# Optimization experiments

Hardware: AMD Instinct MI355X
Metric: run time of the kernel (lower is better)

Reference implementation:

```python
import jax, jax.numpy as jnp
import numpy as np

NUM_REL = 6
EMBED_DIM = 128
B, N = 8, 1024


def _relation_type(dx, dy):
    # Faithful to _get_relation_type's if/elif chain (order matters).
    return jnp.select(
        [dy > 0.5,
         dy < -0.5,
         dx < -0.5,
         dx > 0.5,
         (jnp.abs(dx) < 0.3) & (jnp.abs(dy) < 0.3)],
        [0, 1, 2, 3, 4],
        5,
    )


def setup_inputs() -> dict:
    key = jax.random.key(0)
    k1, k2, k3, k4 = jax.random.split(key, 4)
    symbols = jax.random.normal(k1, (B, N, EMBED_DIM), dtype=jnp.float32)
    positions = jax.random.normal(k2, (B, N, 2), dtype=jnp.float32)
    # 6 Linear(embed_dim, embed_dim) layers, stacked: W [6, D, D] (torch layout: y = x @ W.T + b)
    bound = 1.0 / np.sqrt(EMBED_DIM)
    W = jax.random.uniform(k3, (NUM_REL, EMBED_DIM, EMBED_DIM), dtype=jnp.float32,
                           minval=-bound, maxval=bound)
    b = jax.random.uniform(k4, (NUM_REL, EMBED_DIM), dtype=jnp.float32,
                           minval=-bound, maxval=bound)
    return {"symbols": symbols, "positions": positions, "W": W, "b": b}


def reference(symbols, positions, W, b):
    Bn, Nn, D = symbols.shape
    # dx[b,i,j] = pos[b,j,0] - pos[b,i,0]; dy likewise (source i -> target j)
    dx = positions[:, None, :, 0] - positions[:, :, None, 0]  # [B, i, j]
    dy = positions[:, None, :, 1] - positions[:, :, None, 1]
    rel = _relation_type(dx, dy)  # [B, i, j] in {0..5}

    # Per-type transform of every source symbol: T[r,b,i,:] = symbols[b,i] @ W[r].T + b[r]
    T = jnp.einsum('bid,red->rbie', symbols, W) + b[:, None, None, :]  # [6, B, N, D]

    # One-hot relation mask with i != j excluded; scatter-add into targets j.
    not_diag = ~jnp.eye(Nn, dtype=bool)  # [i, j]
    mask = (rel[None] == jnp.arange(NUM_REL)[:, None, None, None]) & not_diag  # [6, B, i, j]
    agg = jnp.einsum('rbij,rbie->bje', mask.astype(symbols.dtype), T)  # [B, N, D]
    return symbols + agg
```

## Files before the change

### kernel.cpp

```cpp
#include <hip/hip_runtime.h>
#include <stdint.h>


typedef __attribute__((ext_vector_type(8))) short bf16x8;
typedef __attribute__((ext_vector_type(4))) float f32x4;
union U4B { uint4 u; bf16x8 b; };

#if defined(__has_builtin)
#  if __has_builtin(__builtin_amdgcn_global_load_lds)
#    define HAVE_GLL 1
#  endif
#  if __has_builtin(__builtin_amdgcn_mul_u24)
#    define OH_MUL24 1
#  endif
#endif

__device__ __forceinline__ uint16_t f2bf(float f) {
    union { float f; uint32_t u; } v; v.f = f;
    uint32_t u = v.u;
    uint32_t r = (u + 0x7FFFu + ((u >> 16) & 1u)) >> 16;
    return (uint16_t)r;
}

#define BARRIER_LGKM() do {                                   \
    asm volatile("s_waitcnt lgkmcnt(0)" ::: "memory");        \
    __builtin_amdgcn_s_barrier();                             \
    asm volatile("" ::: "memory");                            \
} while (0)

__global__ __launch_bounds__(256)
void prep_kernel(const float* __restrict__ X, const float* __restrict__ W,
                 uint16_t* __restrict__ symT, uint16_t* __restrict__ WtB,
                 float* __restrict__ T4) {
    const int blk = blockIdx.x, tid = threadIdx.x;
    if (blk < 256) {
        __shared__ float T[64 * 65];
        const int b = blk & 7, z = blk >> 3, it = z & 15, et = z >> 4;
        const int i0 = it * 64, e0 = et * 64;
        const float4* Xf = (const float4*)X;
#pragma unroll
        for (int s = 0; s < 4; ++s) {
            int il = s * 16 + (tid >> 4), e4 = tid & 15;
            float4 v = Xf[((size_t)b << 15) + (size_t)((i0 + il) << 5) + (e0 >> 2) + e4];
            T[il * 65 + e4 * 4 + 0] = v.x;
            T[il * 65 + e4 * 4 + 1] = v.y;
            T[il * 65 + e4 * 4 + 2] = v.z;
            T[il * 65 + e4 * 4 + 3] = v.w;
        }
        __syncthreads();
#pragma unroll
        for (int s = 0; s < 4; ++s) {
            int el = s * 16 + (tid >> 4), il4 = tid & 15;
            uint16_t h0 = f2bf(T[(il4 * 4 + 0) * 65 + el]);
            uint16_t h1 = f2bf(T[(il4 * 4 + 1) * 65 + el]);
            uint16_t h2 = f2bf(T[(il4 * 4 + 2) * 65 + el]);
            uint16_t h3 = f2bf(T[(il4 * 4 + 3) * 65 + el]);
            uint2 pk = { (uint32_t)h0 | ((uint32_t)h1 << 16),
                         (uint32_t)h2 | ((uint32_t)h3 << 16) };
            *(uint2*)&symT[((size_t)b << 17) + ((size_t)(e0 + el) << 10) + i0 + il4 * 4] = pk;
        }
    } else if (blk < 352) {
        int g = (blk - 256) * 256 + tid;
        float4 v = ((const float4*)W)[g];
        int r = g >> 12, rem = g & 4095, ep = rem >> 5, e4 = rem & 31;
        int kb = r * 4 + (e4 >> 3);
        int kc = (e4 & 7) * 4;
        uint16_t h0 = f2bf(v.x), h1 = f2bf(v.y), h2 = f2bf(v.z), h3 = f2bf(v.w);
        uint2 pk = { (uint32_t)h0 | ((uint32_t)h1 << 16),
                     (uint32_t)h2 | ((uint32_t)h3 << 16) };
        *(uint2*)&WtB[((size_t)(kb * 128 + ep)) * 32 + kc] = pk;
    } else {
        const int z = blk - 352, bb = z >> 2, qq = z & 3;
        const int e = tid & 127, half = tid >> 7;
        const float* base = X + (((size_t)(bb << 10) + (qq << 8) + (half << 7)) << 7) + e;
        float s = 0.f;
#pragma unroll 8
        for (int itr = 0; itr < 128; ++itr) s += base[(size_t)itr << 7];
        __shared__ float red[256];
        red[tid] = s;
        __syncthreads();
        if (tid < 128) T4[(z << 7) + tid] = red[tid] + red[tid + 128];
    }
}

#define SP 776

__global__ __launch_bounds__(512, 4)
void fused_kernel(const float* __restrict__ sym, const float* __restrict__ pos,
                  const uint16_t* __restrict__ symT, const uint16_t* __restrict__ WtB,
                  const float* __restrict__ bias, const float* __restrict__ T4,
                  float* __restrict__ out) {
    __shared__ __align__(16) char smem[81920];
    uint16_t* symTS   = (uint16_t*)smem;
    float2*   posS    = (float2*)(smem + 32768);
    uint16_t* SA      = (uint16_t*)smem;
    float*    partial = (float*)(smem + 24832);
    uint32_t* rel32   = (uint32_t*)(smem + 65536);

    const int blk = blockIdx.x;
    const int b = blk & 7, jt = blk >> 3, j0 = jt * 16;
    const int tid = threadIdx.x;
    const int w = tid >> 6, lane = tid & 63, m = lane & 15, q = lane >> 4;

    const uint16_t* symTb = symT + ((size_t)b << 17);

    int goff[4];
#pragma unroll
    for (int s = 0; s < 4; ++s) {
        int e = (w << 4) + (s << 2) + (lane >> 4);
        int sg = (lane & 15) ^ (e & 15);
        goff[s] = (e << 10) + (sg << 3);
    }
    const int lwb = w << 12;

    auto issue_chunk = [&](int cidx, int bufsel) {
#ifdef HAVE_GLL
#pragma unroll
        for (int s = 0; s < 4; ++s) {
            const uint16_t* gp = symTb + goff[s] + cidx * 128;
            char* lp = smem + bufsel * 32768 + lwb + s * 1024;
            typedef const __attribute__((address_space(1))) uint32_t gu32;
            typedef __attribute__((address_space(3))) uint32_t lu32;
            __builtin_amdgcn_global_load_lds((gu32*)gp, (lu32*)lp, 16, 0, 0);
        }
#else
#pragma unroll
        for (int s = 0; s < 4; ++s) {
            uint4 v = *(const uint4*)(symTb + goff[s] + cidx * 128);
            *(uint4*)(smem + bufsel * 32768 + lwb + s * 1024 + lane * 16) = v;
        }
#endif
    };

    const float2* pos2 = (const float2*)pos + ((size_t)b << 10);
    float2 p0 = pos2[tid], p1 = pos2[tid + 512];
    issue_chunk(0, 0);
    posS[tid] = p0;
    posS[tid + 512] = p1;
    BARRIER_LGKM();

    {
        const int mm = tid & 15, grp = tid >> 4;
        const int j = j0 + mm;
        const float2 pj = posS[j];
        uint32_t* dst = &rel32[mm * 256];
        const int sw = mm * 2;
#pragma unroll
        for (int s = 0; s < 8; ++s) {
            uint32_t word = 0;
#pragma unroll
            for (int qq = 0; qq < 4; ++qq) {
                int i = grp * 32 + s * 4 + qq;
                float2 pi = posS[i];
                float dx = pj.x - pi.x, dy = pj.y - pi.y;
                int r = (dy > 0.5f) ? 0
                      : (dy < -0.5f) ? 1
                      : (dx < -0.5f) ? 2
                      : (dx > 0.5f)  ? 3
                      : (fabsf(dx) < 0.3f && fabsf(dy) < 0.3f) ? 4
                      : 5;
                uint32_t oh = (i == j) ? 0u : (1u << r);
                word |= oh << (8 * qq);
            }
            dst[(grp * 8 + s) ^ sw] = word;
        }
    }
    BARRIER_LGKM();

    f32x4 acc[5];
#pragma unroll
    for (int r = 0; r < 5; ++r) acc[r] = (f32x4){0.f, 0.f, 0.f, 0.f};

    const int E = (w << 4) + m;
    const int esw = m;
    const int csw = m * 2;

    for (int c = 0; c < 8; ++c) {
        if (c < 7) {
            issue_chunk(c + 1, (c + 1) & 1);
            asm volatile("s_waitcnt vmcnt(4)" ::: "memory");
        } else {
            asm volatile("s_waitcnt vmcnt(0)" ::: "memory");
        }
        const uint16_t* bt = symTS + ((c & 1) << 14) + E * 128;
        const uint32_t* crow = &rel32[m * 256 + c * 32];
#pragma unroll
        for (int ks = 0; ks < 4; ++ks) {
            U4B bfr;
            bfr.u = *(const uint4*)(bt + ((((ks << 2) + q) ^ esw) << 3));
            uint2 cw = *(const uint2*)&crow[(((ks << 3) + (q << 1)) ^ csw)];
            uint32_t hx01 = __builtin_amdgcn_perm(cw.x, cw.x, 0x01010000u) & 0x00FF00FFu;
            uint32_t hx23 = __builtin_amdgcn_perm(cw.x, cw.x, 0x03030202u) & 0x00FF00FFu;
            uint32_t hy01 = __builtin_amdgcn_perm(cw.y, cw.y, 0x01010000u) & 0x00FF00FFu;
            uint32_t hy23 = __builtin_amdgcn_perm(cw.y, cw.y, 0x03030202u) & 0x00FF00FFu;
#pragma unroll
            for (int r = 0; r < 5; ++r) {
                const uint32_t rm = 0x00010001u << r;
                U4B a;
#ifdef OH_MUL24
                const uint32_t mc = 0x3F80u >> r;
                a.u.x = (uint32_t)__builtin_amdgcn_mul_u24((int)(hx01 & rm), (int)mc);
                a.u.y = (uint32_t)__builtin_amdgcn_mul_u24((int)(hx23 & rm), (int)mc);
                a.u.z = (uint32_t)__builtin_amdgcn_mul_u24((int)(hy01 & rm), (int)mc);
                a.u.w = (uint32_t)__builtin_amdgcn_mul_u24((int)(hy23 & rm), (int)mc);
#else
                uint32_t g2;
                g2 = hx01 & rm; a.u.x = (g2 << (14 - r)) - (g2 << (7 - r));
                g2 = hx23 & rm; a.u.y = (g2 << (14 - r)) - (g2 << (7 - r));
                g2 = hy01 & rm; a.u.z = (g2 << (14 - r)) - (g2 << (7 - r));
                g2 = hy23 & rm; a.u.w = (g2 << (14 - r)) - (g2 << (7 - r));
#endif
                acc[r] = __builtin_amdgcn_mfma_f32_16x16x32_bf16(a.b, bfr.b, acc[r], 0, 0, 0);
            }
        }
    }
    BARRIER_LGKM();

#pragma unroll
    for (int r = 0; r < 5; ++r)
#pragma unroll
        for (int reg = 0; reg < 4; ++reg)
            SA[(q * 4 + reg) * SP + r * 128 + E] = f2bf(acc[r][reg]);
    {
        float ts = T4[((b << 2) + 0) * 128 + E] + T4[((b << 2) + 1) * 128 + E]
                 + T4[((b << 2) + 2) * 128 + E] + T4[((b << 2) + 3) * 128 + E];
#pragma unroll
        for (int reg = 0; reg < 4; ++reg) {
            float symj = sym[((size_t)((b << 10) + j0 + (q << 2) + reg) << 7) + E];
            float s5 = ts - symj
                     - acc[0][reg] - acc[1][reg] - acc[2][reg] - acc[3][reg] - acc[4][reg];
            SA[(q * 4 + reg) * SP + 5 * 128 + E] = f2bf(s5);
        }
    }
    BARRIER_LGKM();

    {
        const int g = w >> 1, h = w & 1;
        f32x4 c2[4];
#pragma unroll
        for (int nf = 0; nf < 4; ++nf) c2[nf] = (f32x4){0.f, 0.f, 0.f, 0.f};
#pragma unroll
        for (int kf = 0; kf < 6; ++kf) {
            U4B af;
            af.u = *(const uint4*)&SA[m * SP + g * 192 + kf * 32 + q * 8];
            const int kb = g * 6 + kf;
#pragma unroll
            for (int nf = 0; nf < 4; ++nf) {
                U4B bw;
                bw.u = *(const uint4*)&WtB[((size_t)(kb * 128 + h * 64 + nf * 16 + m)) * 32 + q * 8];
                c2[nf] = __builtin_amdgcn_mfma_f32_16x16x32_bf16(af.b, bw.b, c2[nf], 0, 0, 0);
            }
        }
#pragma unroll
        for (int nf = 0; nf < 4; ++nf)
#pragma unroll
            for (int reg = 0; reg < 4; ++reg)
                partial[g * 2112 + (q * 4 + reg) * 132 + h * 64 + nf * 16 + m] = c2[nf][reg];
    }
    BARRIER_LGKM();

    {
        const int j = tid >> 5, t = tid & 31, e0 = t << 2;
        const uint32_t* row = &rel32[j * 256 + t * 8];
        uint32_t s0 = 0, s1 = 0, s2 = 0, s3 = 0, s4 = 0;
#pragma unroll
        for (int k = 0; k < 8; ++k) {
            uint32_t wd = row[k];
            s0 += wd & 0x01010101u;        s1 += (wd >> 1) & 0x01010101u;
            s2 += (wd >> 2) & 0x01010101u; s3 += (wd >> 3) & 0x01010101u;
            s4 += (wd >> 4) & 0x01010101u;
        }
        int cnt[6];
        cnt[0] = (int)((s0 * 0x01010101u) >> 24);
        cnt[1] = (int)((s1 * 0x01010101u) >> 24);
        cnt[2] = (int)((s2 * 0x01010101u) >> 24);
        cnt[3] = (int)((s3 * 0x01010101u) >> 24);
        cnt[4] = (int)((s4 * 0x01010101u) >> 24);
#pragma unroll
        for (int off = 1; off < 32; off <<= 1)
#pragma unroll
            for (int r = 0; r < 5; ++r)
                cnt[r] += __shfl_xor(cnt[r], off, 64);
        cnt[5] = 1023 - cnt[0] - cnt[1] - cnt[2] - cnt[3] - cnt[4];

        float4 a4 = {0.f, 0.f, 0.f, 0.f};
#pragma unroll
        for (int g4 = 0; g4 < 4; ++g4) {
            float4 u = *(const float4*)&partial[g4 * 2112 + j * 132 + e0];
            a4.x += u.x; a4.y += u.y; a4.z += u.z; a4.w += u.w;
        }
#pragma unroll
        for (int r = 0; r < 6; ++r) {
            float cf = (float)cnt[r];
            float4 bb = *(const float4*)&bias[r * 128 + e0];
            a4.x += cf * bb.x; a4.y += cf * bb.y; a4.z += cf * bb.z; a4.w += cf * bb.w;
        }
        size_t o = ((size_t)(b * 1024 + j0 + j) << 7) + e0;
        float4 sv = *(const float4*)&sym[o];
        float4 ov = { sv.x + a4.x, sv.y + a4.y, sv.z + a4.z, sv.w + a4.w };
        *(float4*)&out[o] = ov;
    }
}

extern "C" void kernel_launch(void* const* d_in, const int* in_sizes, int n_in,
                              void* d_out, int out_size, void* d_ws, size_t ws_size,
                              hipStream_t stream) {
    const float* symbols   = (const float*)d_in[0];
    const float* positions = (const float*)d_in[1];
    const float* W         = (const float*)d_in[2];
    const float* bias      = (const float*)d_in[3];
    float* out             = (float*)d_out;

    char* ws = (char*)d_ws;
    uint16_t* symT = (uint16_t*)ws;
    uint16_t* WtB  = (uint16_t*)(ws + 2097152);
    float*    T4   = (float*)(ws + 2097152 + 196608);

    prep_kernel<<<384, 256, 0, stream>>>(symbols, W, symT, WtB, T4);
    fused_kernel<<<512, 512, 0, stream>>>(symbols, positions, symT, WtB, bias, T4, out);
}
```

Baseline: 94.00 us.

## Precompute one-hot A fragments in shared memory and halve K-chunk size

Moves the one-hot relation-mask expansion out of the MFMA inner loop. Each chunk's bf16 A fragments are now built once per block into a double-buffered LDS region, instead of every wave redundantly expanding them from packed bytes. The K loop is split into 16 chunks of 64 rows rather than 8 chunks of 128, with a new XOR swizzle, and the total shared memory footprint shrinks. In exchange, every chunk now ends with a block-wide barrier and the inner loop adds extra LDS reads for the A fragments.

```diff
diff --git a/kernel.cpp b/kernel.cpp
--- a/kernel.cpp
+++ b/kernel.cpp
@@ -90,12 +90,11 @@
                   const uint16_t* __restrict__ symT, const uint16_t* __restrict__ WtB,
                   const float* __restrict__ bias, const float* __restrict__ T4,
                   float* __restrict__ out) {
-    __shared__ __align__(16) char smem[81920];
-    uint16_t* symTS   = (uint16_t*)smem;
+    __shared__ __align__(16) char smem[75008];
     float2*   posS    = (float2*)(smem + 32768);
     uint16_t* SA      = (uint16_t*)smem;
     float*    partial = (float*)(smem + 24832);
-    uint32_t* rel32   = (uint32_t*)(smem + 65536);
+    uint32_t* rel32   = (uint32_t*)(smem + 58624);
 
     const int blk = blockIdx.x;
     const int b = blk & 7, jt = blk >> 3, j0 = jt * 16;
@@ -104,37 +103,79 @@
 
     const uint16_t* symTb = symT + ((size_t)b << 17);
 
-    int goff[4];
-#pragma unroll
-    for (int s = 0; s < 4; ++s) {
-        int e = (w << 4) + (s << 2) + (lane >> 4);
-        int sg = (lane & 15) ^ (e & 15);
-        goff[s] = (e << 10) + (sg << 3);
-    }
-    const int lwb = w << 12;
+    int goff[2];
+#pragma unroll
+    for (int s = 0; s < 2; ++s) {
+        int e = (w << 4) + (s << 3) + (lane >> 3);
+        int t = lane & 7;
+        goff[s] = (e << 10) + ((t ^ (e & 7)) << 3);
+    }
 
     auto issue_chunk = [&](int cidx, int bufsel) {
 #ifdef HAVE_GLL
 #pragma unroll
-        for (int s = 0; s < 4; ++s) {
-            const uint16_t* gp = symTb + goff[s] + cidx * 128;
-            char* lp = smem + bufsel * 32768 + lwb + s * 1024;
+        for (int s = 0; s < 2; ++s) {
+            const uint16_t* gp = symTb + goff[s] + cidx * 64;
+            char* lp = smem + bufsel * 16384 + (w << 11) + (s << 10);
             typedef const __attribute__((address_space(1))) uint32_t gu32;
             typedef __attribute__((address_space(3))) uint32_t lu32;
             __builtin_amdgcn_global_load_lds((gu32*)gp, (lu32*)lp, 16, 0, 0);
         }
 #else
 #pragma unroll
-        for (int s = 0; s < 4; ++s) {
-            uint4 v = *(const uint4*)(symTb + goff[s] + cidx * 128);
-            *(uint4*)(smem + bufsel * 32768 + lwb + s * 1024 + lane * 16) = v;
+        for (int s = 0; s < 2; ++s) {
+            uint4 v = *(const uint4*)(symTb + goff[s] + cidx * 64);
+            *(uint4*)(smem + bufsel * 16384 + (w << 11) + (s << 10) + lane * 16) = v;
         }
 #endif
     };
 
+    const int jx = tid & 15, u16 = (tid >> 4) & 15, rsub = tid >> 8;
+    const int aseg = (u16 >> 1) ^ (jx & 7), ahb = (u16 & 1) * 8;
+
+    auto expandA = [&](int cidx, int bufsel) {
+        uint32_t cw4 = rel32[jx * 256 + (((cidx << 4) + u16) ^ (jx << 1))];
+        uint32_t h01 = __builtin_amdgcn_perm(cw4, cw4, 0x01010000u) & 0x00FF00FFu;
+        uint32_t h23 = __builtin_amdgcn_perm(cw4, cw4, 0x03030202u) & 0x00FF00FFu;
+        char* ab = smem + 32768 + bufsel * 10240;
+        if (rsub == 0) {
+#pragma unroll
+            for (int r = 0; r < 3; ++r) {
+                const uint32_t rm = 0x00010001u << r;
+                uint2 d;
+#ifdef OH_MUL24
+                const uint32_t mc = 0x3F80u >> r;
+                d.x = (uint32_t)__builtin_amdgcn_mul_u24((int)(h01 & rm), (int)mc);
+                d.y = (uint32_t)__builtin_amdgcn_mul_u24((int)(h23 & rm), (int)mc);
+#else
+                uint32_t g2;
+                g2 = h01 & rm; d.x = (g2 << (14 - r)) - (g2 << (7 - r));
+                g2 = h23 & rm; d.y = (g2 << (14 - r)) - (g2 << (7 - r));
+#endif
+                *(uint2*)(ab + (((r * 16 + jx) * 8 + aseg) << 4) + ahb) = d;
+            }
+        } else {
+#pragma unroll
+            for (int r = 3; r < 5; ++r) {
+                const uint32_t rm = 0x00010001u << r;
+                uint2 d;
+#ifdef OH_MUL24
+                const uint32_t mc = 0x3F80u >> r;
+                d.x = (uint32_t)__builtin_amdgcn_mul_u24((int)(h01 & rm), (int)mc);
+                d.y = (uint32_t)__builtin_amdgcn_mul_u24((int)(h23 & rm), (int)mc);
+#else
+                uint32_t g2;
+                g2 = h01 & rm; d.x = (g2 << (14 - r)) - (g2 << (7 - r));
+                g2 = h23 & rm; d.y = (g2 << (14 - r)) - (g2 << (7 - r));
+#endif
+                *(uint2*)(ab + (((r * 16 + jx) * 8 + aseg) << 4) + ahb) = d;
+            }
+        }
+    };
+
+    issue_chunk(0, 0);
     const float2* pos2 = (const float2*)pos + ((size_t)b << 10);
     float2 p0 = pos2[tid], p1 = pos2[tid + 512];
-    issue_chunk(0, 0);
     posS[tid] = p0;
     posS[tid + 512] = p1;
     BARRIER_LGKM();
@@ -167,54 +208,42 @@
     }
     BARRIER_LGKM();
 
+    expandA(0, 0);
+    BARRIER_LGKM();
+
     f32x4 acc[5];
 #pragma unroll
     for (int r = 0; r < 5; ++r) acc[r] = (f32x4){0.f, 0.f, 0.f, 0.f};
 
     const int E = (w << 4) + m;
-    const int esw = m;
-    const int csw = m * 2;
-
-    for (int c = 0; c < 8; ++c) {
-        if (c < 7) {
-            issue_chunk(c + 1, (c + 1) & 1);
-            asm volatile("s_waitcnt vmcnt(4)" ::: "memory");
+    const int bseg0 = q ^ (m & 7);
+    const int bseg1 = (4 + q) ^ (m & 7);
+
+    for (int c = 0; c < 16; ++c) {
+        const int cb = c & 1;
+        if (c < 15) {
+            issue_chunk(c + 1, cb ^ 1);
+            expandA(c + 1, cb ^ 1);
+            asm volatile("s_waitcnt vmcnt(2)" ::: "memory");
         } else {
             asm volatile("s_waitcnt vmcnt(0)" ::: "memory");
         }
-        const uint16_t* bt = symTS + ((c & 1) << 14) + E * 128;
-        const uint32_t* crow = &rel32[m * 256 + c * 32];
-#pragma unroll
-        for (int ks = 0; ks < 4; ++ks) {
+        const char* bb = smem + cb * 16384 + (w << 11) + (m << 7);
+        const char* ab = smem + 32768 + cb * 10240;
+#pragma unroll
+        for (int ks = 0; ks < 2; ++ks) {
             U4B bfr;
-            bfr.u = *(const uint4*)(bt + ((((ks << 2) + q) ^ esw) << 3));
-            uint2 cw = *(const uint2*)&crow[(((ks << 3) + (q << 1)) ^ csw)];
-            uint32_t hx01 = __builtin_amdgcn_perm(cw.x, cw.x, 0x01010000u) & 0x00FF00FFu;
-            uint32_t hx23 = __builtin_amdgcn_perm(cw.x, cw.x, 0x03030202u) & 0x00FF00FFu;
-            uint32_t hy01 = __builtin_amdgcn_perm(cw.y, cw.y, 0x01010000u) & 0x00FF00FFu;
-            uint32_t hy23 = __builtin_amdgcn_perm(cw.y, cw.y, 0x03030202u) & 0x00FF00FFu;
+            bfr.u = *(const uint4*)(bb + ((ks ? bseg1 : bseg0) << 4));
 #pragma unroll
             for (int r = 0; r < 5; ++r) {
-                const uint32_t rm = 0x00010001u << r;
-                U4B a;
-#ifdef OH_MUL24
-                const uint32_t mc = 0x3F80u >> r;
-                a.u.x = (uint32_t)__builtin_amdgcn_mul_u24((int)(hx01 & rm), (int)mc);
-                a.u.y = (uint32_t)__builtin_amdgcn_mul_u24((int)(hx23 & rm), (int)mc);
-                a.u.z = (uint32_t)__builtin_amdgcn_mul_u24((int)(hy01 & rm), (int)mc);
-                a.u.w = (uint32_t)__builtin_amdgcn_mul_u24((int)(hy23 & rm), (int)mc);
-#else
-                uint32_t g2;
-                g2 = hx01 & rm; a.u.x = (g2 << (14 - r)) - (g2 << (7 - r));
-                g2 = hx23 & rm; a.u.y = (g2 << (14 - r)) - (g2 << (7 - r));
-                g2 = hy01 & rm; a.u.z = (g2 << (14 - r)) - (g2 << (7 - r));
-                g2 = hy23 & rm; a.u.w = (g2 << (14 - r)) - (g2 << (7 - r));
-#endif
-                acc[r] = __builtin_amdgcn_mfma_f32_16x16x32_bf16(a.b, bfr.b, acc[r], 0, 0, 0);
-            }
-        }
-    }
-    BARRIER_LGKM();
+                U4B afr;
+                afr.u = *(const uint4*)(ab + ((((r * 16 + m) * 8) +
+                                               (ks ? bseg1 : bseg0)) << 4));
+                acc[r] = __builtin_amdgcn_mfma_f32_16x16x32_bf16(afr.b, bfr.b, acc[r], 0, 0, 0);
+            }
+        }
+        BARRIER_LGKM();
+    }
 
 #pragma unroll
     for (int r = 0; r < 5; ++r)
```

Result: no change. 93.88 us (-0.1%).

## Shrink LDS footprint with smaller chunks and fuse second GEMM epilogue

Applied to the files above, without the earlier changes.

Halves the symT streaming chunk (64 columns, 16 chunks instead of 8) so the double buffer uses 16KB per buffer, cutting shared memory from 80KB to about 48KB so more blocks can be resident per CU. The second GEMM is restructured so each wave owns 16 output columns over the full K=768, which removes the cross-wave partial-sum buffer and its extra barrier, and the output is written directly from MFMA registers. Relation counts are computed before the main loop and stored in LDS. The trade-offs are more loop iterations and waits per chunk, and scalar rather than float4 stores for the output.

```diff
diff --git a/kernel.cpp b/kernel.cpp
--- a/kernel.cpp
+++ b/kernel.cpp
@@ -86,16 +86,15 @@
 #define SP 776
 
 __global__ __launch_bounds__(512, 4)
-void fused_kernel(const float* __restrict__ sym, const float* __restrict__ pos,
+void fused_kernel(const float* __restrict__ X, const float* __restrict__ pos,
                   const uint16_t* __restrict__ symT, const uint16_t* __restrict__ WtB,
                   const float* __restrict__ bias, const float* __restrict__ T4,
                   float* __restrict__ out) {
-    __shared__ __align__(16) char smem[81920];
-    uint16_t* symTS   = (uint16_t*)smem;
-    float2*   posS    = (float2*)(smem + 32768);
-    uint16_t* SA      = (uint16_t*)smem;
-    float*    partial = (float*)(smem + 24832);
-    uint32_t* rel32   = (uint32_t*)(smem + 65536);
+    __shared__ __align__(16) char smem[49536];
+    float2*   posS  = (float2*)(smem + 16384);
+    uint16_t* SA    = (uint16_t*)smem;
+    uint32_t* rel32 = (uint32_t*)(smem + 32768);
+    float*    cntL  = (float*)(smem + 49152);
 
     const int blk = blockIdx.x;
     const int b = blk & 7, jt = blk >> 3, j0 = jt * 16;
@@ -104,37 +103,36 @@
 
     const uint16_t* symTb = symT + ((size_t)b << 17);
 
-    int goff[4];
-#pragma unroll
-    for (int s = 0; s < 4; ++s) {
-        int e = (w << 4) + (s << 2) + (lane >> 4);
-        int sg = (lane & 15) ^ (e & 15);
-        goff[s] = (e << 10) + (sg << 3);
-    }
-    const int lwb = w << 12;
+    int goff[2];
+#pragma unroll
+    for (int s = 0; s < 2; ++s) {
+        int e = (w << 4) + (s << 3) + (lane >> 3);
+        int t = lane & 7;
+        goff[s] = (e << 10) + ((t ^ (e & 7)) << 3);
+    }
 
     auto issue_chunk = [&](int cidx, int bufsel) {
 #ifdef HAVE_GLL
 #pragma unroll
-        for (int s = 0; s < 4; ++s) {
-            const uint16_t* gp = symTb + goff[s] + cidx * 128;
-            char* lp = smem + bufsel * 32768 + lwb + s * 1024;
+        for (int s = 0; s < 2; ++s) {
+            const uint16_t* gp = symTb + goff[s] + cidx * 64;
+            char* lp = smem + bufsel * 16384 + (w << 11) + (s << 10);
             typedef const __attribute__((address_space(1))) uint32_t gu32;
             typedef __attribute__((address_space(3))) uint32_t lu32;
             __builtin_amdgcn_global_load_lds((gu32*)gp, (lu32*)lp, 16, 0, 0);
         }
 #else
 #pragma unroll
-        for (int s = 0; s < 4; ++s) {
-            uint4 v = *(const uint4*)(symTb + goff[s] + cidx * 128);
-            *(uint4*)(smem + bufsel * 32768 + lwb + s * 1024 + lane * 16) = v;
+        for (int s = 0; s < 2; ++s) {
+            uint4 v = *(const uint4*)(symTb + goff[s] + cidx * 64);
+            *(uint4*)(smem + bufsel * 16384 + (w << 11) + (s << 10) + lane * 16) = v;
         }
 #endif
     };
 
+    issue_chunk(0, 0);
     const float2* pos2 = (const float2*)pos + ((size_t)b << 10);
     float2 p0 = pos2[tid], p1 = pos2[tid + 512];
-    issue_chunk(0, 0);
     posS[tid] = p0;
     posS[tid + 512] = p1;
     BARRIER_LGKM();
@@ -167,28 +165,58 @@
     }
     BARRIER_LGKM();
 
+    {
+        const int j = tid >> 5, t = tid & 31;
+        const uint32_t* row = &rel32[j * 256 + t * 8];
+        uint32_t s0 = 0, s1 = 0, s2 = 0, s3 = 0, s4 = 0;
+#pragma unroll
+        for (int k = 0; k < 8; ++k) {
+            uint32_t wd = row[k];
+            s0 += wd & 0x01010101u;        s1 += (wd >> 1) & 0x01010101u;
+            s2 += (wd >> 2) & 0x01010101u; s3 += (wd >> 3) & 0x01010101u;
+            s4 += (wd >> 4) & 0x01010101u;
+        }
+        int cnt[6];
+        cnt[0] = (int)((s0 * 0x01010101u) >> 24);
+        cnt[1] = (int)((s1 * 0x01010101u) >> 24);
+        cnt[2] = (int)((s2 * 0x01010101u) >> 24);
+        cnt[3] = (int)((s3 * 0x01010101u) >> 24);
+        cnt[4] = (int)((s4 * 0x01010101u) >> 24);
+#pragma unroll
+        for (int off = 1; off < 32; off <<= 1)
+#pragma unroll
+            for (int r = 0; r < 5; ++r)
+                cnt[r] += __shfl_xor(cnt[r], off, 64);
+        if (t == 0) {
+#pragma unroll
+            for (int r = 0; r < 5; ++r) cntL[j * 6 + r] = (float)cnt[r];
+            cntL[j * 6 + 5] = (float)(1023 - cnt[0] - cnt[1] - cnt[2] - cnt[3] - cnt[4]);
+        }
+    }
+
     f32x4 acc[5];
 #pragma unroll
     for (int r = 0; r < 5; ++r) acc[r] = (f32x4){0.f, 0.f, 0.f, 0.f};
 
     const int E = (w << 4) + m;
-    const int esw = m;
-    const int csw = m * 2;
-
-    for (int c = 0; c < 8; ++c) {
-        if (c < 7) {
+    const int bseg0 = q ^ (m & 7);
+    const int bseg1 = (4 + q) ^ (m & 7);
+    const int csw = m << 1;
+
+    for (int c = 0; c < 16; ++c) {
+        if (c < 15) {
             issue_chunk(c + 1, (c + 1) & 1);
-            asm volatile("s_waitcnt vmcnt(4)" ::: "memory");
+            asm volatile("s_waitcnt vmcnt(2)" ::: "memory");
         } else {
             asm volatile("s_waitcnt vmcnt(0)" ::: "memory");
         }
-        const uint16_t* bt = symTS + ((c & 1) << 14) + E * 128;
-        const uint32_t* crow = &rel32[m * 256 + c * 32];
-#pragma unroll
-        for (int ks = 0; ks < 4; ++ks) {
+        const char* bb = smem + (c & 1) * 16384 + (w << 11) + (m << 7);
+#pragma unroll
+        for (int ks = 0; ks < 2; ++ks) {
             U4B bfr;
-            bfr.u = *(const uint4*)(bt + ((((ks << 2) + q) ^ esw) << 3));
-            uint2 cw = *(const uint2*)&crow[(((ks << 3) + (q << 1)) ^ csw)];
+            bfr.u = *(const uint4*)(bb + ((ks ? bseg1 : bseg0) << 4));
+            uint2 cw = *(const uint2*)&rel32[m * 256 +
+                           (((c << 4) + (ks << 3) + (q << 1)) ^ csw)];
             uint32_t hx01 = __builtin_amdgcn_perm(cw.x, cw.x, 0x01010000u) & 0x00FF00FFu;
             uint32_t hx23 = __builtin_amdgcn_perm(cw.x, cw.x, 0x03030202u) & 0x00FF00FFu;
             uint32_t hy01 = __builtin_amdgcn_perm(cw.y, cw.y, 0x01010000u) & 0x00FF00FFu;
@@ -226,7 +254,7 @@
                  + T4[((b << 2) + 2) * 128 + E] + T4[((b << 2) + 3) * 128 + E];
 #pragma unroll
         for (int reg = 0; reg < 4; ++reg) {
-            float symj = sym[((size_t)((b << 10) + j0 + (q << 2) + reg) << 7) + E];
+            float symj = X[((size_t)((b << 10) + j0 + (q << 2) + reg) << 7) + E];
             float s5 = ts - symj
                      - acc[0][reg] - acc[1][reg] - acc[2][reg] - acc[3][reg] - acc[4][reg];
             SA[(q * 4 + reg) * SP + 5 * 128 + E] = f2bf(s5);
@@ -235,70 +263,28 @@
     BARRIER_LGKM();
 
     {
-        const int g = w >> 1, h = w & 1;
-        f32x4 c2[4];
-#pragma unroll
-        for (int nf = 0; nf < 4; ++nf) c2[nf] = (f32x4){0.f, 0.f, 0.f, 0.f};
-#pragma unroll
-        for (int kf = 0; kf < 6; ++kf) {
-            U4B af;
-            af.u = *(const uint4*)&SA[m * SP + g * 192 + kf * 32 + q * 8];
-            const int kb = g * 6 + kf;
-#pragma unroll
-            for (int nf = 0; nf < 4; ++nf) {
-                U4B bw;
-                bw.u = *(const uint4*)&WtB[((size_t)(kb * 128 + h * 64 + nf * 16 + m)) * 32 + q * 8];
-                c2[nf] = __builtin_amdgcn_mfma_f32_16x16x32_bf16(af.b, bw.b, c2[nf], 0, 0, 0);
-            }
-        }
-#pragma unroll
-        for (int nf = 0; nf < 4; ++nf)
-#pragma unroll
-            for (int reg = 0; reg < 4; ++reg)
-                partial[g * 2112 + (q * 4 + reg) * 132 + h * 64 + nf * 16 + m] = c2[nf][reg];
-    }
-    BARRIER_LGKM();
-
-    {
-        const int j = tid >> 5, t = tid & 31, e0 = t << 2;
-        const uint32_t* row = &rel32[j * 256 + t * 8];
-        uint32_t s0 = 0, s1 = 0, s2 = 0, s3 = 0, s4 = 0;
-#pragma unroll
-        for (int k = 0; k < 8; ++k) {
-            uint32_t wd = row[k];
-            s0 += wd & 0x01010101u;        s1 += (wd >> 1) & 0x01010101u;
-            s2 += (wd >> 2) & 0x01010101u; s3 += (wd >> 3) & 0x01010101u;
-            s4 += (wd >> 4) & 0x01010101u;
-        }
-        int cnt[6];
-        cnt[0] = (int)((s0 * 0x01010101u) >> 24);
-        cnt[1] = (int)((s1 * 0x01010101u) >> 24);
-        cnt[2] = (int)((s2 * 0x01010101u) >> 24);
-        cnt[3] = (int)((s3 * 0x01010101u) >> 24);
-        cnt[4] = (int)((s4 * 0x01010101u) >> 24);
-#pragma unroll
-        for (int off = 1; off < 32; off <<= 1)
-#pragma unroll
-            for (int r = 0; r < 5; ++r)
-                cnt[r] += __shfl_xor(cnt[r], off, 64);
-        cnt[5] = 1023 - cnt[0] - cnt[1] - cnt[2] - cnt[3] - cnt[4];
-
-        float4 a4 = {0.f, 0.f, 0.f, 0.f};
-#pragma unroll
-        for (int g4 = 0; g4 < 4; ++g4) {
-            float4 u = *(const float4*)&partial[g4 * 2112 + j * 132 + e0];
-            a4.x += u.x; a4.y += u.y; a4.z += u.z; a4.w += u.w;
-        }
-#pragma unroll
-        for (int r = 0; r < 6; ++r) {
-            float cf = (float)cnt[r];
-            float4 bb = *(const float4*)&bias[r * 128 + e0];
-            a4.x += cf * bb.x; a4.y += cf * bb.y; a4.z += cf * bb.z; a4.w += cf * bb.w;
-        }
-        size_t o = ((size_t)(b * 1024 + j0 + j) << 7) + e0;
-        float4 sv = *(const float4*)&sym[o];
-        float4 ov = { sv.x + a4.x, sv.y + a4.y, sv.z + a4.z, sv.w + a4.w };
-        *(float4*)&out[o] = ov;
+        f32x4 c3 = (f32x4){0.f, 0.f, 0.f, 0.f};
+#pragma unroll
+        for (int kb = 0; kb < 24; ++kb) {
+            U4B af, bw;
+            af.u = *(const uint4*)&SA[m * SP + kb * 32 + q * 8];
+            bw.u = *(const uint4*)&WtB[((size_t)(kb * 128 + (w << 4) + m)) * 32 + q * 8];
+            c3 = __builtin_amdgcn_mfma_f32_16x16x32_bf16(af.b, bw.b, c3, 0, 0, 0);
+        }
+
+        const int e = (w << 4) + m;
+        float be[6];
+#pragma unroll
+        for (int r = 0; r < 6; ++r) be[r] = bias[r * 128 + e];
+#pragma unroll
+        for (int reg = 0; reg < 4; ++reg) {
+            const int j = q * 4 + reg;
+            float add = c3[reg];
+#pragma unroll
+            for (int r = 0; r < 6; ++r) add += cntL[j * 6 + r] * be[r];
+            size_t o = ((size_t)((b << 10) + j0 + j) << 7) + e;
+            out[o] = X[o] + add;
+        }
     }
 }
 
```

New measurement: 95.45 us. No clear change (+1.5%).
